# Optimization experiments

Measured on AMD Instinct MI355X. Metric: run time of the kernel, lower is better.

The kernel has to match this reference:

```python
import jax, jax.numpy as jnp
import numpy as np


def setup_inputs() -> dict:
    key = jax.random.key(0)
    k1, _ = jax.random.split(key)
    B, S, D = 4, 4096, 64
    inp = jax.random.normal(k1, (B, S, D), dtype=jnp.float32)
    attn_mask = jnp.zeros((S, S), dtype=bool)  # no masked positions
    return {"input": inp, "attn_mask": attn_mask}


def reference(input, attn_mask):
    # attn_mask: bool [S,S] -> additive mask with -inf at masked positions
    am = jnp.where(attn_mask, -jnp.inf, 0.0).T  # transpose(0,1)
    # scores: [B,S,S]
    v = jnp.einsum('bsd,btd->bst', input, input)
    mask = (1.0 - am) * -10000.0
    v = v + mask  # dead in original module too: w is drawn fresh below
    # w = empty_like(v).uniform_(-0.1, 0.1)
    wkey = jax.random.key(42)
    w = jax.random.uniform(wkey, v.shape, dtype=v.dtype, minval=-0.1, maxval=0.1)
    w = jax.nn.softmax(w, axis=-1)
    # per-column (dim 1) L1 renorm: w[:, i] /= ||w[:, i]||_1 over (batch, last dim)
    denom = jnp.sum(jnp.abs(w), axis=(0, 2), keepdims=True)  # [1,S,1]
    w = w / denom
    return jnp.einsum('bst,btd->bsd', w, input)
```

## Files before the change

### kernel.cpp

```cpp
#include <hip/hip_runtime.h>
#include <hip/hip_bf16.h>
#include <stdint.h>


#define S_ 4096
#define D_ 64

typedef __attribute__((ext_vector_type(8))) short short8v;
typedef __attribute__((ext_vector_type(4))) float floatx4;

__device__ __forceinline__ uint32_t rotl32(uint32_t x, unsigned r) {
    return (x << r) | (x >> (32u - r));
}

__device__ __forceinline__ uint32_t threefry_bits(uint32_t f) {
    const uint32_t k0 = 0u, k1 = 42u;
    const uint32_t k2 = 0x1BD11BDAu ^ k0 ^ k1;
    uint32_t x0 = k0;
    uint32_t x1 = f + k1;
#define TFR(r) { x0 += x1; x1 = rotl32(x1, (r)); x1 ^= x0; }
    TFR(13) TFR(15) TFR(26) TFR(6)
    x0 += k1; x1 += k2 + 1u;
    TFR(17) TFR(29) TFR(16) TFR(24)
    x0 += k2; x1 += k0 + 2u;
    TFR(13) TFR(15) TFR(26) TFR(6)
    x0 += k0; x1 += k1 + 3u;
    TFR(17) TFR(29) TFR(16) TFR(24)
    x0 += k1; x1 += k2 + 4u;
    TFR(13) TFR(15) TFR(26) TFR(6)
    x0 += k2; x1 += k0 + 5u;
#undef TFR
    return x0 ^ x1;
}

__device__ __forceinline__ float uniform_exp_poly(uint32_t bits) {
    const float t = __uint_as_float((bits >> 9) | 0x3F800000u);
    const float u = __builtin_fmaf(t, 0.2f, -0.3f);
    float p = __builtin_fmaf(u, 0.16666667f, 0.5f);
    p = __builtin_fmaf(p, u, 1.0f);
    return __builtin_fmaf(p, u, 1.0f);
}

__global__ __launch_bounds__(64) void pack_xt_bf16(
    const float* __restrict__ x, short* __restrict__ bf)
{
    const int id = blockIdx.x;
    const int l  = threadIdx.x;
    const int kc = id & 127;
    const int dg = (id >> 7) & 3;
    const int b  = id >> 9;
    const int d  = dg * 16 + (l & 15);
    const int k0 = kc * 32 + (l >> 4) * 8;
    const float* __restrict__ xb = x + (size_t)b * (S_ * D_);
    union { short8v v; short s[8]; } r;
#pragma unroll
    for (int j = 0; j < 8; ++j) {
        __hip_bfloat16 h = __float2bfloat16(xb[(size_t)(k0 + j) * D_ + d]);
        r.s[j] = __builtin_bit_cast(short, h);
    }
    *(short8v*)&bf[(size_t)id * 512 + l * 8] = r.v;
}

__global__ __launch_bounds__(256, 4) void fused_rand_attn_mfma2(
    const short* __restrict__ bf, float* __restrict__ out)
{
    const int tid  = threadIdx.x;
    const int bid  = (blockIdx.x & 7) * 128 + (blockIdx.x >> 3);
    const int b    = bid >> 8;
    const int s0   = (bid & 255) * 16;
    const int w    = tid >> 6;
    const int lane = tid & 63;
    const int lt   = lane & 15;
    const int lh   = lane >> 4;

    __shared__ float ACC[4][4][64][4];
    __shared__ float ZL[4][16];

    floatx4 acc0 = {0.f,0.f,0.f,0.f}, acc1 = {0.f,0.f,0.f,0.f};
    floatx4 acc2 = {0.f,0.f,0.f,0.f}, acc3 = {0.f,0.f,0.f,0.f};
    float zp = 0.f;

    const short* __restrict__ bfb = bf + (size_t)b * (4 * 128 * 512);
    const uint32_t fbase = ((uint32_t)b << 24) | ((uint32_t)(s0 + lt) << 12);

#pragma unroll 1
    for (int kt = w; kt < 64; kt += 4) {
        short8v bfr[8];
#pragma unroll
        for (int dg = 0; dg < 4; ++dg)
#pragma unroll
            for (int kc = 0; kc < 2; ++kc)
                bfr[dg * 2 + kc] = *(const short8v*)
                    &bfb[(size_t)((dg * 128 + kt * 2 + kc) * 512 + lane * 8)];

        union { uint32_t u[4]; short8v v; } a0, a1;
#pragma unroll
        for (int kc = 0; kc < 2; ++kc) {
            const uint32_t kb = fbase + (uint32_t)(kt * 64 + kc * 32 + lh * 8);
#pragma unroll
            for (int jp = 0; jp < 4; ++jp) {
                const float e0 = uniform_exp_poly(threefry_bits(kb + 2 * jp));
                const float e1 = uniform_exp_poly(threefry_bits(kb + 2 * jp + 1));
                zp += e0 + e1;
                const uint32_t u0 = __float_as_uint(e0) + 0x8000u;
                const uint32_t u1 = __float_as_uint(e1) + 0x8000u;
                const uint32_t pk = (u0 >> 16) | (u1 & 0xFFFF0000u);
                if (kc == 0) a0.u[jp] = pk; else a1.u[jp] = pk;
            }
        }

        acc0 = __builtin_amdgcn_mfma_f32_16x16x32_bf16(a0.v, bfr[0], acc0, 0,0,0);
        acc0 = __builtin_amdgcn_mfma_f32_16x16x32_bf16(a1.v, bfr[1], acc0, 0,0,0);
        acc1 = __builtin_amdgcn_mfma_f32_16x16x32_bf16(a0.v, bfr[2], acc1, 0,0,0);
        acc1 = __builtin_amdgcn_mfma_f32_16x16x32_bf16(a1.v, bfr[3], acc1, 0,0,0);
        acc2 = __builtin_amdgcn_mfma_f32_16x16x32_bf16(a0.v, bfr[4], acc2, 0,0,0);
        acc2 = __builtin_amdgcn_mfma_f32_16x16x32_bf16(a1.v, bfr[5], acc2, 0,0,0);
        acc3 = __builtin_amdgcn_mfma_f32_16x16x32_bf16(a0.v, bfr[6], acc3, 0,0,0);
        acc3 = __builtin_amdgcn_mfma_f32_16x16x32_bf16(a1.v, bfr[7], acc3, 0,0,0);
    }

    zp += __shfl_xor(zp, 16);
    zp += __shfl_xor(zp, 32);
    if (lane < 16) ZL[w][lane] = zp;
    *(floatx4*)&ACC[w][0][lane][0] = acc0;
    *(floatx4*)&ACC[w][1][lane][0] = acc1;
    *(floatx4*)&ACC[w][2][lane][0] = acc2;
    *(floatx4*)&ACC[w][3][lane][0] = acc3;
    __syncthreads();

    floatx4 facc = {0.f,0.f,0.f,0.f};
#pragma unroll
    for (int w2 = 0; w2 < 4; ++w2) {
        const floatx4 t = *(const floatx4*)&ACC[w2][w][lane][0];
        facc.x += t.x; facc.y += t.y; facc.z += t.z; facc.w += t.w;
    }
    const int col = w * 16 + lt;
#pragma unroll
    for (int r = 0; r < 4; ++r) {
        const int row = lh * 4 + r;
        const float Z = ZL[0][row] + ZL[1][row] + ZL[2][row] + ZL[3][row];
        const float scale = 1.0f / (4.0f * Z);
        out[((size_t)b * S_ + (s0 + row)) * D_ + col] = facc[r] * scale;
    }
}

extern "C" void kernel_launch(void* const* d_in, const int* in_sizes, int n_in,
                              void* d_out, int out_size, void* d_ws, size_t ws_size,
                              hipStream_t stream) {
    const float* x = (const float*)d_in[0];
    float* out = (float*)d_out;
    short* bfw = (short*)d_ws;
    (void)in_sizes; (void)n_in; (void)out_size; (void)ws_size;
    hipLaunchKernelGGL(pack_xt_bf16, dim3(2048), dim3(64), 0, stream, x, bfw);
    hipLaunchKernelGGL(fused_rand_attn_mfma2, dim3(1024), dim3(256), 0, stream,
                       bfw, out);
}
```

Measured before the change: 141.8 us.

## Use 8 waves per block, hardware bf16 pack, and interleave loads with RNG

The fused kernel goes from 4 to 8 waves per block, so each wave handles half as many key tiles, and the cross-wave shared-memory reduction is widened to match. The manual round-to-nearest bf16 packing becomes a single v_cvt_pk_bf16_f32 instruction. B-operand loads are split and interleaved with the Threefry generation and the MFMAs to hide latency. The softmax sum uses two accumulators. More waves raise shared-memory use and the launch bound asks for higher occupancy, which may cause register spills.

```diff
diff --git a/kernel.cpp b/kernel.cpp
--- a/kernel.cpp
+++ b/kernel.cpp
@@ -41,6 +41,25 @@
     return __builtin_fmaf(p, u, 1.0f);
 }
 
+__device__ __forceinline__ uint32_t cvt_pk_bf16(float e0, float e1) {
+    uint32_t r;
+    asm("v_cvt_pk_bf16_f32 %0, %1, %2" : "=v"(r) : "v"(e0), "v"(e1));
+    return r;
+}
+
+__device__ __forceinline__ short8v gen_a(uint32_t c0, float& zpA, float& zpB) {
+    union { uint32_t u[4]; short8v v; } a;
+#pragma unroll
+    for (int jp = 0; jp < 4; ++jp) {
+        const float e0 = uniform_exp_poly(threefry_bits(c0 + 2u * jp));
+        const float e1 = uniform_exp_poly(threefry_bits(c0 + 2u * jp + 1u));
+        zpA += e0;
+        zpB += e1;
+        a.u[jp] = cvt_pk_bf16(e0, e1);
+    }
+    return a.v;
+}
+
 __global__ __launch_bounds__(64) void pack_xt_bf16(
     const float* __restrict__ x, short* __restrict__ bf)
 {
@@ -61,7 +80,7 @@
     *(short8v*)&bf[(size_t)id * 512 + l * 8] = r.v;
 }
 
-__global__ __launch_bounds__(256, 4) void fused_rand_attn_mfma2(
+__global__ __launch_bounds__(512, 6) void fused_rand_attn_mfma3(
     const short* __restrict__ bf, float* __restrict__ out)
 {
     const int tid  = threadIdx.x;
@@ -73,52 +92,49 @@
     const int lt   = lane & 15;
     const int lh   = lane >> 4;
 
-    __shared__ float ACC[4][4][64][4];
-    __shared__ float ZL[4][16];
+    __shared__ float ACC[8][4][64][4];
+    __shared__ float ZL[8][16];
 
     floatx4 acc0 = {0.f,0.f,0.f,0.f}, acc1 = {0.f,0.f,0.f,0.f};
     floatx4 acc2 = {0.f,0.f,0.f,0.f}, acc3 = {0.f,0.f,0.f,0.f};
-    float zp = 0.f;
+    float zpA = 0.f, zpB = 0.f;
 
-    const short* __restrict__ bfb = bf + (size_t)b * (4 * 128 * 512);
-    const uint32_t fbase = ((uint32_t)b << 24) | ((uint32_t)(s0 + lt) << 12);
+    const short* __restrict__ bl =
+        bf + (size_t)b * (4 * 128 * 512) + (size_t)lane * 8;
+    const uint32_t fl = (((uint32_t)b << 24) | ((uint32_t)(s0 + lt) << 12))
+                        + (uint32_t)(lh * 8);
 
 #pragma unroll 1
-    for (int kt = w; kt < 64; kt += 4) {
-        short8v bfr[8];
-#pragma unroll
-        for (int dg = 0; dg < 4; ++dg)
-#pragma unroll
-            for (int kc = 0; kc < 2; ++kc)
-                bfr[dg * 2 + kc] = *(const short8v*)
-                    &bfb[(size_t)((dg * 128 + kt * 2 + kc) * 512 + lane * 8)];
+    for (int kt = w; kt < 64; kt += 8) {
+        const short* pk = bl + (size_t)kt * 1024;
+        const uint32_t kb = fl + ((uint32_t)kt << 6);
 
-        union { uint32_t u[4]; short8v v; } a0, a1;
-#pragma unroll
-        for (int kc = 0; kc < 2; ++kc) {
-            const uint32_t kb = fbase + (uint32_t)(kt * 64 + kc * 32 + lh * 8);
-#pragma unroll
-            for (int jp = 0; jp < 4; ++jp) {
-                const float e0 = uniform_exp_poly(threefry_bits(kb + 2 * jp));
-                const float e1 = uniform_exp_poly(threefry_bits(kb + 2 * jp + 1));
-                zp += e0 + e1;
-                const uint32_t u0 = __float_as_uint(e0) + 0x8000u;
-                const uint32_t u1 = __float_as_uint(e1) + 0x8000u;
-                const uint32_t pk = (u0 >> 16) | (u1 & 0xFFFF0000u);
-                if (kc == 0) a0.u[jp] = pk; else a1.u[jp] = pk;
-            }
-        }
+        const short8v b00 = *(const short8v*)(pk);
+        const short8v b10 = *(const short8v*)(pk + 65536);
+        const short8v b20 = *(const short8v*)(pk + 131072);
+        const short8v b30 = *(const short8v*)(pk + 196608);
 
-        acc0 = __builtin_amdgcn_mfma_f32_16x16x32_bf16(a0.v, bfr[0], acc0, 0,0,0);
-        acc0 = __builtin_amdgcn_mfma_f32_16x16x32_bf16(a1.v, bfr[1], acc0, 0,0,0);
-        acc1 = __builtin_amdgcn_mfma_f32_16x16x32_bf16(a0.v, bfr[2], acc1, 0,0,0);
-        acc1 = __builtin_amdgcn_mfma_f32_16x16x32_bf16(a1.v, bfr[3], acc1, 0,0,0);
-        acc2 = __builtin_amdgcn_mfma_f32_16x16x32_bf16(a0.v, bfr[4], acc2, 0,0,0);
-        acc2 = __builtin_amdgcn_mfma_f32_16x16x32_bf16(a1.v, bfr[5], acc2, 0,0,0);
-        acc3 = __builtin_amdgcn_mfma_f32_16x16x32_bf16(a0.v, bfr[6], acc3, 0,0,0);
-        acc3 = __builtin_amdgcn_mfma_f32_16x16x32_bf16(a1.v, bfr[7], acc3, 0,0,0);
+        const short8v a0 = gen_a(kb, zpA, zpB);
+
+        const short8v b01 = *(const short8v*)(pk + 512);
+        const short8v b11 = *(const short8v*)(pk + 65536 + 512);
+        const short8v b21 = *(const short8v*)(pk + 131072 + 512);
+        const short8v b31 = *(const short8v*)(pk + 196608 + 512);
+
+        acc0 = __builtin_amdgcn_mfma_f32_16x16x32_bf16(a0, b00, acc0, 0, 0, 0);
+        acc1 = __builtin_amdgcn_mfma_f32_16x16x32_bf16(a0, b10, acc1, 0, 0, 0);
+        acc2 = __builtin_amdgcn_mfma_f32_16x16x32_bf16(a0, b20, acc2, 0, 0, 0);
+        acc3 = __builtin_amdgcn_mfma_f32_16x16x32_bf16(a0, b30, acc3, 0, 0, 0);
+
+        const short8v a1 = gen_a(kb + 32u, zpA, zpB);
+
+        acc0 = __builtin_amdgcn_mfma_f32_16x16x32_bf16(a1, b01, acc0, 0, 0, 0);
+        acc1 = __builtin_amdgcn_mfma_f32_16x16x32_bf16(a1, b11, acc1, 0, 0, 0);
+        acc2 = __builtin_amdgcn_mfma_f32_16x16x32_bf16(a1, b21, acc2, 0, 0, 0);
+        acc3 = __builtin_amdgcn_mfma_f32_16x16x32_bf16(a1, b31, acc3, 0, 0, 0);
     }
 
+    float zp = zpA + zpB;
     zp += __shfl_xor(zp, 16);
     zp += __shfl_xor(zp, 32);
     if (lane < 16) ZL[w][lane] = zp;
@@ -128,20 +144,26 @@
     *(floatx4*)&ACC[w][3][lane][0] = acc3;
     __syncthreads();
 
+    const int dg = w & 3;
+    const int rh = w >> 2;
     floatx4 facc = {0.f,0.f,0.f,0.f};
 #pragma unroll
-    for (int w2 = 0; w2 < 4; ++w2) {
-        const floatx4 t = *(const floatx4*)&ACC[w2][w][lane][0];
+    for (int w2 = 0; w2 < 8; ++w2) {
+        const floatx4 t = *(const floatx4*)&ACC[w2][dg][lane][0];
         facc.x += t.x; facc.y += t.y; facc.z += t.z; facc.w += t.w;
     }
-    const int col = w * 16 + lt;
+    const float v0 = rh ? facc.z : facc.x;
+    const float v1 = rh ? facc.w : facc.y;
+    const int row0 = lh * 4 + rh * 2;
+    float Z0 = 0.f, Z1 = 0.f;
 #pragma unroll
-    for (int r = 0; r < 4; ++r) {
-        const int row = lh * 4 + r;
-        const float Z = ZL[0][row] + ZL[1][row] + ZL[2][row] + ZL[3][row];
-        const float scale = 1.0f / (4.0f * Z);
-        out[((size_t)b * S_ + (s0 + row)) * D_ + col] = facc[r] * scale;
+    for (int w2 = 0; w2 < 8; ++w2) {
+        Z0 += ZL[w2][row0];
+        Z1 += ZL[w2][row0 + 1];
     }
+    const int col = dg * 16 + lt;
+    out[((size_t)b * S_ + (s0 + row0)) * D_ + col]     = v0 * (0.25f / Z0);
+    out[((size_t)b * S_ + (s0 + row0 + 1)) * D_ + col] = v1 * (0.25f / Z1);
 }
 
 extern "C" void kernel_launch(void* const* d_in, const int* in_sizes, int n_in,
@@ -152,6 +174,6 @@
     short* bfw = (short*)d_ws;
     (void)in_sizes; (void)n_in; (void)out_size; (void)ws_size;
     hipLaunchKernelGGL(pack_xt_bf16, dim3(2048), dim3(64), 0, stream, x, bfw);
-    hipLaunchKernelGGL(fused_rand_attn_mfma2, dim3(1024), dim3(256), 0, stream,
+    hipLaunchKernelGGL(fused_rand_attn_mfma3, dim3(1024), dim3(512), 0, stream,
                        bfw, out);
 }
```

Result: faster. 133.2 us (-6.1%).
